# Performance work log

Hardware: AMD Instinct MI355X
Metric: run time of the kernel (lower is better)

The kernel has to match this reference:

```python
import jax, jax.numpy as jnp
import numpy as np

B, V, C, NB, KS, OUT = 2, 20000, 32, 12, 9, 32


def setup_inputs() -> dict:
    key = jax.random.key(0)
    k1, k2, k3, k4 = jax.random.split(key, 4)
    x = jax.random.normal(k1, (B, V, C), jnp.float32)
    # padded neighbor table: index 0 == padding row, valid indices 1..V
    adj = jax.random.randint(k2, (V, NB), 0, V + 1, dtype=jnp.int32)
    # GlorotNormal-ish scales
    W = jax.random.normal(k3, (C, KS, OUT), jnp.float32) * np.float32(np.sqrt(2.0 / (C + KS * OUT)))
    u = jax.random.normal(k4, (C, KS), jnp.float32) * np.float32(np.sqrt(2.0 / (C + KS)))
    c = jnp.zeros((KS,), jnp.float32)
    b = jnp.zeros((OUT,), jnp.float32)
    return {"x": x, "W": W, "u": u, "c": c, "b": b, "adj": adj}


def reference(x, W, u, c, b, adj):
    Bb, Vv, Cc = x.shape
    ks, out = W.shape[1], W.shape[2]
    # inverse neighbor count (0 index means padding); 0 where no neighbors
    deg = jnp.count_nonzero(adj, axis=-1).astype(x.dtype)            # [V]
    inv_deg = jnp.where(deg > 0, 1.0 / deg, jnp.zeros_like(deg))     # [V]

    # wx = x @ reshape(W) -> per-vertex kernelized features
    wx = jnp.einsum('bvc,cko->bvko', x, W)                           # [B,V,ks,out]
    wx_pad = jnp.concatenate([jnp.zeros((Bb, 1, ks, out), x.dtype), wx], axis=1)
    nb_wx = wx_pad[:, adj]                                           # [B,V,nb,ks,out]

    # attention logits: u(x_i) - u(x_j) + c, softmax over kernel axis
    ux = jnp.einsum('bvc,ck->bvk', x, u)                             # [B,V,ks]
    ux_pad = jnp.concatenate([jnp.zeros((Bb, 1, ks), x.dtype), ux], axis=1)
    nb_ux = ux_pad[:, adj]                                           # [B,V,nb,ks]
    q = jax.nn.softmax(ux[:, :, None, :] - nb_ux + c, axis=-1)       # [B,V,nb,ks]

    # softmax-weighted sum over neighbors, then mean (via inv_deg) over kernels
    agg = jnp.einsum('bvnk,bvnko->bvko', q, nb_wx)                   # [B,V,ks,out]
    res = jnp.einsum('bvko,v->bvo', agg, inv_deg) + b                # [B,V,out]
    return jax.nn.relu(res)
```

## Files before the change

### kernel.cpp

```cpp
#include <hip/hip_runtime.h>
#include <math.h>

#define BDIM 256

constexpr int Bc = 2, Vc = 20000, Cc = 32, NBc = 12, KSc = 9, OUTc = 32;
constexpr int NTASK = Bc * Vc;
constexpr int TPG   = 2;
constexpr int NTRIP = NTASK / TPG;
constexpr int GPB   = 8;
constexpr int GRID  = 768;
constexpr int NSLOT = GRID * GPB;
constexpr int WPAD  = 292;
constexpr int UXP   = 12;

__global__ __launch_bounds__(BDIM)
void ux_kernel(const float* __restrict__ x, const float* __restrict__ u,
               float* __restrict__ ux)
{
    __shared__ float us[Cc * KSc];
    for (int i = threadIdx.x; i < Cc * KSc; i += BDIM) us[i] = u[i];
    __syncthreads();

    const int row = blockIdx.x * BDIM + threadIdx.x;
    if (row >= NTASK) return;

    const float4* xr = (const float4*)(x + row * Cc);
    float4 xv[8];
#pragma unroll
    for (int i = 0; i < 8; ++i) xv[i] = xr[i];

    float acc[KSc];
#pragma unroll
    for (int k = 0; k < KSc; ++k) acc[k] = 0.f;
#pragma unroll
    for (int c = 0; c < Cc; ++c) {
        const float xc = ((const float*)xv)[c];
#pragma unroll
        for (int k = 0; k < KSc; ++k) acc[k] = fmaf(xc, us[c * KSc + k], acc[k]);
    }
    float4* o4 = (float4*)(ux + row * UXP);
    o4[0] = make_float4(acc[0], acc[1], acc[2], acc[3]);
    o4[1] = make_float4(acc[4], acc[5], acc[6], acc[7]);
    o4[2] = make_float4(acc[8], 0.f, 0.f, 0.f);
}

__device__ __forceinline__ float reduce32(float (&z)[OUTc], int lane)
{
#pragma unroll
    for (int i = 0; i < 16; ++i) {
        const bool hi = (lane & 16) != 0;
        const float keep = hi ? z[i + 16] : z[i];
        const float send = hi ? z[i] : z[i + 16];
        z[i] = keep + __shfl_xor(send, 16);
    }
#pragma unroll
    for (int i = 0; i < 8; ++i) {
        const bool hi = (lane & 8) != 0;
        const float keep = hi ? z[i + 8] : z[i];
        const float send = hi ? z[i] : z[i + 8];
        z[i] = keep + __shfl_xor(send, 8);
    }
#pragma unroll
    for (int i = 0; i < 4; ++i) {
        const bool hi = (lane & 4) != 0;
        const float keep = hi ? z[i + 4] : z[i];
        const float send = hi ? z[i] : z[i + 4];
        z[i] = keep + __shfl_xor(send, 4);
    }
#pragma unroll
    for (int i = 0; i < 2; ++i) {
        const bool hi = (lane & 2) != 0;
        const float keep = hi ? z[i + 2] : z[i];
        const float send = hi ? z[i] : z[i + 2];
        z[i] = keep + __shfl_xor(send, 2);
    }
    {
        const bool hi = (lane & 1) != 0;
        const float keep = hi ? z[1] : z[0];
        const float send = hi ? z[0] : z[1];
        return keep + __shfl_xor(send, 1);
    }
}

__global__ __launch_bounds__(BDIM, 3)
void fused_kernel(const float* __restrict__ x, const float* __restrict__ W,
                  const float* __restrict__ cvec, const float* __restrict__ bvec,
                  const int* __restrict__ adj, const float* __restrict__ ux,
                  float* __restrict__ out)
{
    __shared__ __align__(16) float Wl[Cc * WPAD];
    __shared__ __align__(16) float qs[GPB][TPG][KSc][NBc];
    __shared__ __align__(16) int   js[GPB][TPG][NBc];

    const int tid  = threadIdx.x;
    const int g    = tid >> 5;
    const int lane = tid & 31;
    const int h    = (tid >> 5) & 1;

    {
        const float4* Wg = (const float4*)W;
        for (int i = tid; i < Cc * KSc * OUTc / 4; i += BDIM) {
            const int fi = i * 4;
            const int c  = fi / (KSc * OUTc);
            const int r  = fi - c * (KSc * OUTc);
            *(float4*)(&Wl[c * WPAD + r]) = Wg[i];
        }
    }
    float ck[KSc];
#pragma unroll
    for (int k = 0; k < KSc; ++k) ck[k] = cvec[k];
    const float bo = bvec[lane];
    __syncthreads();

    const int slot0 = blockIdx.x * GPB + g;

    for (int trip = slot0; trip < NTRIP; trip += NSLOT) {
        const int t0 = trip * TPG;

        bool pred = false;
        if (lane < 2 * NBc) {
            const int t    = (lane >= NBc) ? 1 : 0;
            const int n    = lane - t * NBc;
            const int task = t0 + t;
            const int bb   = (task >= Vc) ? 1 : 0;
            const int v    = task - bb * Vc;
            const int j    = adj[v * NBc + n];
            pred = (j != 0);
            const int row = pred ? (bb * Vc + j - 1) : 0;
            js[g][t][n] = row;
            const float4* uo4 = (const float4*)(ux + task * UXP);
            const float4* un4 = (const float4*)(ux + row * UXP);
            float uo[12], un[12];
            *(float4*)&uo[0] = uo4[0]; *(float4*)&uo[4] = uo4[1]; *(float4*)&uo[8] = uo4[2];
            *(float4*)&un[0] = un4[0]; *(float4*)&un[4] = un4[1]; *(float4*)&un[8] = un4[2];
            float e[KSc];
            float mx = -3.0e38f;
#pragma unroll
            for (int k = 0; k < KSc; ++k) {
                e[k] = uo[k] - un[k] + ck[k];
                mx = fmaxf(mx, e[k]);
            }
            float s = 0.f;
#pragma unroll
            for (int k = 0; k < KSc; ++k) { e[k] = __expf(e[k] - mx); s += e[k]; }
            const float r = pred ? (1.f / s) : 0.f;
#pragma unroll
            for (int k = 0; k < KSc; ++k) qs[g][t][k][n] = e[k] * r;
        }
        const unsigned long long bal = __ballot(pred);
        const unsigned int mg = (unsigned int)(bal >> (h * 32));
        const int deg0 = __popc(mg & 0xFFFu);
        const int deg1 = __popc((mg >> NBc) & 0xFFFu);
        const float inv0 = (deg0 > 0) ? 1.f / (float)deg0 : 0.f;
        const float inv1 = (deg1 > 0) ? 1.f / (float)deg1 : 0.f;

        float y[TPG][KSc];
#pragma unroll
        for (int t = 0; t < TPG; ++t) {
            const int4* jp = (const int4*)&js[g][t][0];
            const int4 ja = jp[0], jb = jp[1], jc = jp[2];
            int rows[NBc];
            rows[0] = ja.x; rows[1] = ja.y; rows[2]  = ja.z; rows[3]  = ja.w;
            rows[4] = jb.x; rows[5] = jb.y; rows[6]  = jb.z; rows[7]  = jb.w;
            rows[8] = jc.x; rows[9] = jc.y; rows[10] = jc.z; rows[11] = jc.w;
            float xs[NBc];
#pragma unroll
            for (int n = 0; n < NBc; ++n) xs[n] = x[rows[n] * Cc + lane];
#pragma unroll
            for (int k = 0; k < KSc; ++k) {
                const float4* qp = (const float4*)&qs[g][t][k][0];
                const float4 qa = qp[0], qb = qp[1], qc = qp[2];
                float acc = 0.f;
                acc = fmaf(qa.x, xs[0], acc);  acc = fmaf(qa.y, xs[1], acc);
                acc = fmaf(qa.z, xs[2], acc);  acc = fmaf(qa.w, xs[3], acc);
                acc = fmaf(qb.x, xs[4], acc);  acc = fmaf(qb.y, xs[5], acc);
                acc = fmaf(qb.z, xs[6], acc);  acc = fmaf(qb.w, xs[7], acc);
                acc = fmaf(qc.x, xs[8], acc);  acc = fmaf(qc.y, xs[9], acc);
                acc = fmaf(qc.z, xs[10], acc); acc = fmaf(qc.w, xs[11], acc);
                y[t][k] = acc;
            }
        }

        float z0[OUTc], z1[OUTc];
#pragma unroll
        for (int o = 0; o < OUTc; ++o) { z0[o] = 0.f; z1[o] = 0.f; }
        const float* wrow = Wl + lane * WPAD;
#pragma unroll
        for (int k = 0; k < KSc; ++k) {
            const float a0 = y[0][k], a1 = y[1][k];
#pragma unroll
            for (int jj = 0; jj < 8; ++jj) {
                const float4 w4 = *(const float4*)(wrow + k * OUTc + jj * 4);
                z0[jj*4+0] = fmaf(a0, w4.x, z0[jj*4+0]);
                z0[jj*4+1] = fmaf(a0, w4.y, z0[jj*4+1]);
                z0[jj*4+2] = fmaf(a0, w4.z, z0[jj*4+2]);
                z0[jj*4+3] = fmaf(a0, w4.w, z0[jj*4+3]);
                z1[jj*4+0] = fmaf(a1, w4.x, z1[jj*4+0]);
                z1[jj*4+1] = fmaf(a1, w4.y, z1[jj*4+1]);
                z1[jj*4+2] = fmaf(a1, w4.z, z1[jj*4+2]);
                z1[jj*4+3] = fmaf(a1, w4.w, z1[jj*4+3]);
            }
        }

        {
            const float s0 = reduce32(z0, lane);
            out[t0 * OUTc + lane] = fmaxf(fmaf(inv0, s0, bo), 0.f);
            const float s1 = reduce32(z1, lane);
            out[(t0 + 1) * OUTc + lane] = fmaxf(fmaf(inv1, s1, bo), 0.f);
        }
    }
}

extern "C" void kernel_launch(void* const* d_in, const int* in_sizes, int n_in,
                              void* d_out, int out_size, void* d_ws, size_t ws_size,
                              hipStream_t stream)
{
    const float* x    = (const float*)d_in[0];
    const float* W    = (const float*)d_in[1];
    const float* u    = (const float*)d_in[2];
    const float* cvec = (const float*)d_in[3];
    const float* bvec = (const float*)d_in[4];
    const int*   adj  = (const int*)d_in[5];
    float* out = (float*)d_out;

    float* ux = (float*)d_ws;

    ux_kernel<<<(NTASK + BDIM - 1) / BDIM, BDIM, 0, stream>>>(x, u, ux);
    fused_kernel<<<GRID, BDIM, 0, stream>>>(x, W, cvec, bvec, adj, ux, out);
}
```

Baseline: 96.07 us.

## Use bf16x3 split MFMA for W projection with 16-task wave tiles

Replaces the per-lane scalar FMA projection through W plus the 32-wide shuffle reduction with MFMA 16x16x32 bf16 instructions. Fp32 accuracy is approximated by splitting both operands into hi/lo bf16 parts and running three MFMAs per product. W is pre-split and swizzled into the MFMA fragment layout by the prep kernel. Each wave now handles 16 tasks, gathering neighbor x rows as float4 vectors and computing degrees directly from adj. The aim is to cut ALU and shuffle cost, at the price of register pressure (occupancy bound lowered to 2) and small precision loss from the bf16 split.

```diff
diff --git a/kernel.cpp b/kernel.cpp
--- a/kernel.cpp
+++ b/kernel.cpp
@@ -3,136 +3,116 @@
 
 #define BDIM 256
 
-constexpr int Bc = 2, Vc = 20000, Cc = 32, NBc = 12, KSc = 9, OUTc = 32;
-constexpr int NTASK = Bc * Vc;
-constexpr int TPG   = 2;
-constexpr int NTRIP = NTASK / TPG;
-constexpr int GPB   = 8;
-constexpr int GRID  = 768;
-constexpr int NSLOT = GRID * GPB;
-constexpr int WPAD  = 292;
+constexpr int Vc = 20000, Cc = 32, NBc = 12, KSc = 9, OUTc = 32;
+constexpr int NTASK = 40000;
 constexpr int UXP   = 12;
+constexpr int MT    = 16;
+constexpr int NITER = NTASK / MT;
+constexpr int NBLK  = 512;
+constexpr int NWAVE = NBLK * 4;
+constexpr int WFE   = KSc * 2 * 64 * 8;
+
+typedef __attribute__((ext_vector_type(8))) short short8;
+typedef __attribute__((ext_vector_type(4))) float floatx4;
 
 __global__ __launch_bounds__(BDIM)
-void ux_kernel(const float* __restrict__ x, const float* __restrict__ u,
-               float* __restrict__ ux)
+void prep_kernel(const float* __restrict__ x, const float* __restrict__ u,
+                 const float* __restrict__ W, float* __restrict__ ux,
+                 unsigned short* __restrict__ wf)
 {
-    __shared__ float us[Cc * KSc];
-    for (int i = threadIdx.x; i < Cc * KSc; i += BDIM) us[i] = u[i];
-    __syncthreads();
-
-    const int row = blockIdx.x * BDIM + threadIdx.x;
-    if (row >= NTASK) return;
-
-    const float4* xr = (const float4*)(x + row * Cc);
-    float4 xv[8];
-#pragma unroll
-    for (int i = 0; i < 8; ++i) xv[i] = xr[i];
-
-    float acc[KSc];
-#pragma unroll
-    for (int k = 0; k < KSc; ++k) acc[k] = 0.f;
-#pragma unroll
-    for (int c = 0; c < Cc; ++c) {
-        const float xc = ((const float*)xv)[c];
-#pragma unroll
-        for (int k = 0; k < KSc; ++k) acc[k] = fmaf(xc, us[c * KSc + k], acc[k]);
-    }
-    float4* o4 = (float4*)(ux + row * UXP);
-    o4[0] = make_float4(acc[0], acc[1], acc[2], acc[3]);
-    o4[1] = make_float4(acc[4], acc[5], acc[6], acc[7]);
-    o4[2] = make_float4(acc[8], 0.f, 0.f, 0.f);
-}
-
-__device__ __forceinline__ float reduce32(float (&z)[OUTc], int lane)
-{
-#pragma unroll
-    for (int i = 0; i < 16; ++i) {
-        const bool hi = (lane & 16) != 0;
-        const float keep = hi ? z[i + 16] : z[i];
-        const float send = hi ? z[i] : z[i + 16];
-        z[i] = keep + __shfl_xor(send, 16);
-    }
-#pragma unroll
-    for (int i = 0; i < 8; ++i) {
-        const bool hi = (lane & 8) != 0;
-        const float keep = hi ? z[i + 8] : z[i];
-        const float send = hi ? z[i] : z[i + 8];
-        z[i] = keep + __shfl_xor(send, 8);
-    }
-#pragma unroll
-    for (int i = 0; i < 4; ++i) {
-        const bool hi = (lane & 4) != 0;
-        const float keep = hi ? z[i + 4] : z[i];
-        const float send = hi ? z[i] : z[i + 4];
-        z[i] = keep + __shfl_xor(send, 4);
-    }
-#pragma unroll
-    for (int i = 0; i < 2; ++i) {
-        const bool hi = (lane & 2) != 0;
-        const float keep = hi ? z[i + 2] : z[i];
-        const float send = hi ? z[i] : z[i + 2];
-        z[i] = keep + __shfl_xor(send, 2);
-    }
-    {
-        const bool hi = (lane & 1) != 0;
-        const float keep = hi ? z[1] : z[0];
-        const float send = hi ? z[0] : z[1];
-        return keep + __shfl_xor(send, 1);
+    if (blockIdx.x < 157) {
+        __shared__ float us[Cc * KSc];
+        for (int i = threadIdx.x; i < Cc * KSc; i += BDIM) us[i] = u[i];
+        __syncthreads();
+        const int row = blockIdx.x * BDIM + threadIdx.x;
+        if (row >= NTASK) return;
+        const float4* xr = (const float4*)(x + row * Cc);
+        float4 xv[8];
+#pragma unroll
+        for (int i = 0; i < 8; ++i) xv[i] = xr[i];
+        float acc[KSc];
+#pragma unroll
+        for (int k = 0; k < KSc; ++k) acc[k] = 0.f;
+#pragma unroll
+        for (int c = 0; c < Cc; ++c) {
+            const float xc = ((const float*)xv)[c];
+#pragma unroll
+            for (int k = 0; k < KSc; ++k) acc[k] = fmaf(xc, us[c * KSc + k], acc[k]);
+        }
+        float4* o4 = (float4*)(ux + row * UXP);
+        o4[0] = make_float4(acc[0], acc[1], acc[2], acc[3]);
+        o4[1] = make_float4(acc[4], acc[5], acc[6], acc[7]);
+        o4[2] = make_float4(acc[8], 0.f, 0.f, 0.f);
+    } else {
+        const int e = (blockIdx.x - 157) * BDIM + threadIdx.x;
+        if (e >= WFE) return;
+        const int j = e & 7;
+        const int l = (e >> 3) & 63;
+        const int h = (e >> 9) & 1;
+        const int k = e >> 10;
+        const int c = (l >> 4) * 8 + j;
+        const int o = (l & 15) + 16 * h;
+        const float w = W[(c * KSc + k) * OUTc + o];
+        const unsigned int bits = __float_as_uint(w);
+        const unsigned short hi = (unsigned short)(bits >> 16);
+        const float hif = __uint_as_float(bits & 0xFFFF0000u);
+        const float lof = w - hif;
+        const unsigned short lo = (unsigned short)(__float_as_uint(lof) >> 16);
+        wf[e]       = hi;
+        wf[WFE + e] = lo;
     }
 }
 
-__global__ __launch_bounds__(BDIM, 3)
-void fused_kernel(const float* __restrict__ x, const float* __restrict__ W,
-                  const float* __restrict__ cvec, const float* __restrict__ bvec,
-                  const int* __restrict__ adj, const float* __restrict__ ux,
+__global__ __launch_bounds__(BDIM, 2)
+void fused_kernel(const float* __restrict__ x, const float* __restrict__ cvec,
+                  const float* __restrict__ bvec, const int* __restrict__ adj,
+                  const float* __restrict__ ux, const unsigned short* __restrict__ wf,
                   float* __restrict__ out)
 {
-    __shared__ __align__(16) float Wl[Cc * WPAD];
-    __shared__ __align__(16) float qs[GPB][TPG][KSc][NBc];
-    __shared__ __align__(16) int   js[GPB][TPG][NBc];
-
-    const int tid  = threadIdx.x;
-    const int g    = tid >> 5;
-    const int lane = tid & 31;
-    const int h    = (tid >> 5) & 1;
-
+    __shared__ __align__(16) unsigned short wsh[2 * WFE];
+    __shared__ __align__(16) float qs[4][MT][KSc][NBc];
+    __shared__ __align__(16) int   js[4][MT][NBc];
+    __shared__ float invs[4][MT];
+
+    const int tid = threadIdx.x;
     {
-        const float4* Wg = (const float4*)W;
-        for (int i = tid; i < Cc * KSc * OUTc / 4; i += BDIM) {
-            const int fi = i * 4;
-            const int c  = fi / (KSc * OUTc);
-            const int r  = fi - c * (KSc * OUTc);
-            *(float4*)(&Wl[c * WPAD + r]) = Wg[i];
-        }
+        const uint4* src = (const uint4*)wf;
+        uint4* dst = (uint4*)wsh;
+        for (int i = tid; i < (2 * WFE) / 8; i += BDIM) dst[i] = src[i];
     }
     float ck[KSc];
 #pragma unroll
     for (int k = 0; k < KSc; ++k) ck[k] = cvec[k];
-    const float bo = bvec[lane];
+    const int l64 = tid & 63;
+    const int w   = tid >> 6;
+    const int oo  = l64 & 15;
+    const int cb  = l64 >> 4;
+    const float b0 = bvec[oo], b1 = bvec[oo + 16];
     __syncthreads();
 
-    const int slot0 = blockIdx.x * GPB + g;
-
-    for (int trip = slot0; trip < NTRIP; trip += NSLOT) {
-        const int t0 = trip * TPG;
-
-        bool pred = false;
-        if (lane < 2 * NBc) {
-            const int t    = (lane >= NBc) ? 1 : 0;
-            const int n    = lane - t * NBc;
+    const int gw = blockIdx.x * 4 + w;
+    for (int it = gw; it < NITER; it += NWAVE) {
+        const int t0 = it * MT;
+
+#pragma unroll
+        for (int p = 0; p < 3; ++p) {
+            const int unit = p * 64 + l64;
+            const int t    = (unit * 171) >> 11;
+            const int n    = unit - t * 12;
             const int task = t0 + t;
             const int bb   = (task >= Vc) ? 1 : 0;
             const int v    = task - bb * Vc;
-            const int j    = adj[v * NBc + n];
-            pred = (j != 0);
-            const int row = pred ? (bb * Vc + j - 1) : 0;
-            js[g][t][n] = row;
-            const float4* uo4 = (const float4*)(ux + task * UXP);
-            const float4* un4 = (const float4*)(ux + row * UXP);
+            const int jn   = adj[v * NBc + n];
+            const bool pred = (jn != 0);
+            const int row = pred ? (bb * Vc + jn - 1) : 0;
+            js[w][t][n] = row;
             float uo[12], un[12];
-            *(float4*)&uo[0] = uo4[0]; *(float4*)&uo[4] = uo4[1]; *(float4*)&uo[8] = uo4[2];
-            *(float4*)&un[0] = un4[0]; *(float4*)&un[4] = un4[1]; *(float4*)&un[8] = un4[2];
+            {
+                const float4* uo4 = (const float4*)(ux + task * UXP);
+                const float4* un4 = (const float4*)(ux + row * UXP);
+                *(float4*)&uo[0] = uo4[0]; *(float4*)&uo[4] = uo4[1]; *(float4*)&uo[8] = uo4[2];
+                *(float4*)&un[0] = un4[0]; *(float4*)&un[4] = un4[1]; *(float4*)&un[8] = un4[2];
+            }
             float e[KSc];
             float mx = -3.0e38f;
 #pragma unroll
@@ -145,68 +125,91 @@
             for (int k = 0; k < KSc; ++k) { e[k] = __expf(e[k] - mx); s += e[k]; }
             const float r = pred ? (1.f / s) : 0.f;
 #pragma unroll
-            for (int k = 0; k < KSc; ++k) qs[g][t][k][n] = e[k] * r;
-        }
-        const unsigned long long bal = __ballot(pred);
-        const unsigned int mg = (unsigned int)(bal >> (h * 32));
-        const int deg0 = __popc(mg & 0xFFFu);
-        const int deg1 = __popc((mg >> NBc) & 0xFFFu);
-        const float inv0 = (deg0 > 0) ? 1.f / (float)deg0 : 0.f;
-        const float inv1 = (deg1 > 0) ? 1.f / (float)deg1 : 0.f;
-
-        float y[TPG][KSc];
-#pragma unroll
-        for (int t = 0; t < TPG; ++t) {
-            const int4* jp = (const int4*)&js[g][t][0];
+            for (int k = 0; k < KSc; ++k) qs[w][t][k][n] = e[k] * r;
+        }
+        if (l64 < MT) {
+            const int task = t0 + l64;
+            const int bb   = (task >= Vc) ? 1 : 0;
+            const int v    = task - bb * Vc;
+            const int4* ar = (const int4*)(adj + v * NBc);
+            const int4 a0 = ar[0], a1 = ar[1], a2 = ar[2];
+            const int d = (a0.x != 0) + (a0.y != 0) + (a0.z != 0) + (a0.w != 0)
+                        + (a1.x != 0) + (a1.y != 0) + (a1.z != 0) + (a1.w != 0)
+                        + (a2.x != 0) + (a2.y != 0) + (a2.z != 0) + (a2.w != 0);
+            invs[w][l64] = (d > 0) ? 1.f / (float)d : 0.f;
+        }
+
+        const int tA = l64 & 15;
+        float y[KSc][8];
+#pragma unroll
+        for (int k = 0; k < KSc; ++k)
+#pragma unroll
+            for (int j = 0; j < 8; ++j) y[k][j] = 0.f;
+
+        int rows[NBc];
+        {
+            const int4* jp = (const int4*)&js[w][tA][0];
             const int4 ja = jp[0], jb = jp[1], jc = jp[2];
-            int rows[NBc];
             rows[0] = ja.x; rows[1] = ja.y; rows[2]  = ja.z; rows[3]  = ja.w;
             rows[4] = jb.x; rows[5] = jb.y; rows[6]  = jb.z; rows[7]  = jb.w;
             rows[8] = jc.x; rows[9] = jc.y; rows[10] = jc.z; rows[11] = jc.w;
-            float xs[NBc];
-#pragma unroll
-            for (int n = 0; n < NBc; ++n) xs[n] = x[rows[n] * Cc + lane];
+        }
+#pragma unroll
+        for (int nb = 0; nb < 3; ++nb) {
+            float xs[4][8];
+#pragma unroll
+            for (int i = 0; i < 4; ++i) {
+                const float4* xp = (const float4*)(x + rows[nb * 4 + i] * Cc + cb * 8);
+                *(float4*)&xs[i][0] = xp[0];
+                *(float4*)&xs[i][4] = xp[1];
+            }
 #pragma unroll
             for (int k = 0; k < KSc; ++k) {
-                const float4* qp = (const float4*)&qs[g][t][k][0];
-                const float4 qa = qp[0], qb = qp[1], qc = qp[2];
-                float acc = 0.f;
-                acc = fmaf(qa.x, xs[0], acc);  acc = fmaf(qa.y, xs[1], acc);
-                acc = fmaf(qa.z, xs[2], acc);  acc = fmaf(qa.w, xs[3], acc);
-                acc = fmaf(qb.x, xs[4], acc);  acc = fmaf(qb.y, xs[5], acc);
-                acc = fmaf(qb.z, xs[6], acc);  acc = fmaf(qb.w, xs[7], acc);
-                acc = fmaf(qc.x, xs[8], acc);  acc = fmaf(qc.y, xs[9], acc);
-                acc = fmaf(qc.z, xs[10], acc); acc = fmaf(qc.w, xs[11], acc);
-                y[t][k] = acc;
-            }
-        }
-
-        float z0[OUTc], z1[OUTc];
-#pragma unroll
-        for (int o = 0; o < OUTc; ++o) { z0[o] = 0.f; z1[o] = 0.f; }
-        const float* wrow = Wl + lane * WPAD;
+                const float4 q4 = *(const float4*)&qs[w][tA][k][nb * 4];
+#pragma unroll
+                for (int j = 0; j < 8; ++j) {
+                    float a = y[k][j];
+                    a = fmaf(q4.x, xs[0][j], a);
+                    a = fmaf(q4.y, xs[1][j], a);
+                    a = fmaf(q4.z, xs[2][j], a);
+                    a = fmaf(q4.w, xs[3][j], a);
+                    y[k][j] = a;
+                }
+            }
+        }
+
+        floatx4 acc0 = {0.f, 0.f, 0.f, 0.f};
+        floatx4 acc1 = {0.f, 0.f, 0.f, 0.f};
 #pragma unroll
         for (int k = 0; k < KSc; ++k) {
-            const float a0 = y[0][k], a1 = y[1][k];
-#pragma unroll
-            for (int jj = 0; jj < 8; ++jj) {
-                const float4 w4 = *(const float4*)(wrow + k * OUTc + jj * 4);
-                z0[jj*4+0] = fmaf(a0, w4.x, z0[jj*4+0]);
-                z0[jj*4+1] = fmaf(a0, w4.y, z0[jj*4+1]);
-                z0[jj*4+2] = fmaf(a0, w4.z, z0[jj*4+2]);
-                z0[jj*4+3] = fmaf(a0, w4.w, z0[jj*4+3]);
-                z1[jj*4+0] = fmaf(a1, w4.x, z1[jj*4+0]);
-                z1[jj*4+1] = fmaf(a1, w4.y, z1[jj*4+1]);
-                z1[jj*4+2] = fmaf(a1, w4.z, z1[jj*4+2]);
-                z1[jj*4+3] = fmaf(a1, w4.w, z1[jj*4+3]);
-            }
-        }
-
-        {
-            const float s0 = reduce32(z0, lane);
-            out[t0 * OUTc + lane] = fmaxf(fmaf(inv0, s0, bo), 0.f);
-            const float s1 = reduce32(z1, lane);
-            out[(t0 + 1) * OUTc + lane] = fmaxf(fmaf(inv1, s1, bo), 0.f);
+            short8 ah, al;
+#pragma unroll
+            for (int j = 0; j < 8; ++j) {
+                const unsigned int yb = __float_as_uint(y[k][j]);
+                ah[j] = (short)(yb >> 16);
+                const float hif = __uint_as_float(yb & 0xFFFF0000u);
+                const float lof = y[k][j] - hif;
+                al[j] = (short)(__float_as_uint(lof) >> 16);
+            }
+            const short8 bh0 = *(const short8*)&wsh[((k * 2 + 0) * 64 + l64) * 8];
+            const short8 bh1 = *(const short8*)&wsh[((k * 2 + 1) * 64 + l64) * 8];
+            const short8 bl0 = *(const short8*)&wsh[WFE + ((k * 2 + 0) * 64 + l64) * 8];
+            const short8 bl1 = *(const short8*)&wsh[WFE + ((k * 2 + 1) * 64 + l64) * 8];
+            acc0 = __builtin_amdgcn_mfma_f32_16x16x32_bf16(ah, bh0, acc0, 0, 0, 0);
+            acc0 = __builtin_amdgcn_mfma_f32_16x16x32_bf16(al, bh0, acc0, 0, 0, 0);
+            acc0 = __builtin_amdgcn_mfma_f32_16x16x32_bf16(ah, bl0, acc0, 0, 0, 0);
+            acc1 = __builtin_amdgcn_mfma_f32_16x16x32_bf16(ah, bh1, acc1, 0, 0, 0);
+            acc1 = __builtin_amdgcn_mfma_f32_16x16x32_bf16(al, bh1, acc1, 0, 0, 0);
+            acc1 = __builtin_amdgcn_mfma_f32_16x16x32_bf16(ah, bl1, acc1, 0, 0, 0);
+        }
+
+#pragma unroll
+        for (int r = 0; r < 4; ++r) {
+            const int tl   = cb * 4 + r;
+            const float nv = invs[w][tl];
+            const int task = t0 + tl;
+            out[task * OUTc + oo]      = fmaxf(fmaf(acc0[r], nv, b0), 0.f);
+            out[task * OUTc + oo + 16] = fmaxf(fmaf(acc1[r], nv, b1), 0.f);
         }
     }
 }
@@ -223,8 +226,9 @@
     const int*   adj  = (const int*)d_in[5];
     float* out = (float*)d_out;
 
-    float* ux = (float*)d_ws;
-
-    ux_kernel<<<(NTASK + BDIM - 1) / BDIM, BDIM, 0, stream>>>(x, u, ux);
-    fused_kernel<<<GRID, BDIM, 0, stream>>>(x, W, cvec, bvec, adj, ux, out);
+    float*          ux = (float*)d_ws;
+    unsigned short* wf = (unsigned short*)((char*)d_ws + 1920000);
+
+    prep_kernel<<<157 + 36, BDIM, 0, stream>>>(x, u, W, ux, wf);
+    fused_kernel<<<NBLK, BDIM, 0, stream>>>(x, cvec, bvec, adj, ux, wf, out);
 }
```

Result: no change. 96.28 us (+0.2%).
